# Kernel optimization log

Measured on AMD Instinct MI355X. Metric: run time of the kernel, lower is better.

Reference implementation:

```python
import jax, jax.numpy as jnp
import numpy as np
from jax import lax

T = 8192
D_MODEL = 768
D_RNN = 1024
KW = 4  # conv kernel width


def setup_inputs() -> dict:
    key = jax.random.key(0)
    ks = jax.random.split(key, 9)
    x = jax.random.normal(ks[0], (T, D_MODEL), jnp.float32)
    # equinox nn.Linear(in, out): weight [out, in], bias [out]
    w1 = jax.random.normal(ks[1], (2 * D_RNN, D_MODEL), jnp.float32) / np.sqrt(D_MODEL)
    b1 = jnp.zeros((2 * D_RNN,), jnp.float32)
    # nn.Conv1d(d_rnn, d_rnn, 4, use_bias=False): kernel [out_ch, in_ch, kw]
    conv_w = jax.random.normal(ks[2], (D_RNN, D_RNN, KW), jnp.float32) / np.sqrt(D_RNN * KW)
    w_rg = jax.random.normal(ks[3], (2 * D_RNN, D_RNN), jnp.float32) / np.sqrt(D_RNN)
    b_rg = jnp.zeros((2 * D_RNN,), jnp.float32)
    w_out = jax.random.normal(ks[4], (D_MODEL, D_RNN), jnp.float32) / np.sqrt(D_RNN)
    b_out = jnp.zeros((D_MODEL,), jnp.float32)
    # Lambda ~ U(inv_sigmoid(0.9)^{1/8}, inv_sigmoid(0.999)^{1/8}) as in __init__
    inv_sig = lambda p: np.log(1.0 / (1.0 - p))
    lower = np.power(inv_sig(0.9), 1.0 / 8.0)
    upper = np.power(inv_sig(0.999), 1.0 / 8.0)
    Lambda = jax.random.uniform(ks[5], (D_RNN,), jnp.float32, lower, upper)
    return {"x": x, "w1": w1, "b1": b1, "conv_w": conv_w, "w_rg": w_rg,
            "b_rg": b_rg, "w_out": w_out, "b_out": b_out, "Lambda": Lambda}


def _rglru_forward(x, w1, b1, conv_w, w_rg, b_rg, w_out, b_out, Lambda):
    # lin1 then split into gate branch (gelu) and recurrent branch
    h = x @ w1.T + b1                       # [T, 2*D_RNN]
    a_branch = jax.nn.gelu(h[:, :D_RNN])    # [T, D_RNN]
    b_branch = h[:, D_RNN:]                 # [T, D_RNN]
    # causal conv1d: lhs [N=1, C, T], rhs [O, I, KW], left pad 3
    bc = lax.conv_general_dilated(b_branch.T[None], conv_w, (1,), [(KW - 1, 0)])[0].T  # [T, D_RNN]
    # RG-LRU gating
    g = jax.nn.sigmoid(bc @ w_rg.T + b_rg)  # [T, 2*D_RNN]
    inp_gate = g[:, :D_RNN]
    rec_gate = g[:, D_RNN:]
    a_t = jnp.exp(-8.0 * jax.nn.softplus(Lambda)[None, :] * rec_gate)  # [T, D_RNN]
    gated_x = jnp.sqrt(1.0 - a_t ** 2) * inp_gate * bc

    def rec_step(state, xs):
        gx, av = xs
        hn = av * state + gx
        return hn, hn

    _, y = lax.scan(rec_step, jnp.zeros((D_RNN,), x.dtype), (gated_x, a_t))
    return (a_branch * y) @ w_out.T + b_out  # [T, D_MODEL]


def reference(x, w1, b1, conv_w, w_rg, b_rg, w_out, b_out, Lambda):
    return _rglru_forward(x, w1, b1, conv_w, w_rg, b_rg, w_out, b_out, Lambda)
```

## Files before the change

kernel.cpp:

```cpp
#include <hip/hip_runtime.h>
#include <hip/hip_bf16.h>
#include <stdint.h>


#define T_LEN 8192
#define DM 768
#define DR 1024
#define NC 128
#define CL 64

typedef __bf16 bf16x8 __attribute__((ext_vector_type(8)));
typedef float  f32x4  __attribute__((ext_vector_type(4)));

#define AS1 __attribute__((address_space(1)))
#define AS3 __attribute__((address_space(3)))

__device__ __forceinline__ void cp16_g2l(const void* g, void* l) {
    __builtin_amdgcn_global_load_lds((const AS1 void*)g, (AS3 void*)l, 16, 0, 0);
}

__device__ __forceinline__ float gelu_tanh(float x) {
    const float inner = 0.7978845608028654f * (x + 0.044715f * x * x * x);
    return 0.5f * x * (1.f + tanhf(inner));
}

template<int BN, int EPI, bool SHIFT>
__global__ __launch_bounds__(256, 2)
void gemm_mfma(const __hip_bfloat16* __restrict__ A,
               const __hip_bfloat16* __restrict__ B,
               const float* __restrict__ bias,
               void* __restrict__ Cv,
               int K, int lda, int N,
               __hip_bfloat16* __restrict__ D2)
{
    constexpr int NI  = BN / 32;
    constexpr int NLD = 4 + NI;
    __shared__ __bf16 As[2][128 * 64];
    __shared__ __bf16 Bs[2][BN * 64];

    const int tid  = threadIdx.x;
    const int lane = tid & 63;
    const int wave = tid >> 6;
    const size_t m0 = (size_t)blockIdx.x * 128;
    const int    n0 = blockIdx.y * BN;
    const int wm = (wave >> 1) * 64;
    const int wn = (wave & 1) * (BN / 2);

    f32x4 acc[4][NI];
#pragma unroll
    for (int i = 0; i < 4; ++i)
#pragma unroll
        for (int j = 0; j < NI; ++j)
            acc[i][j] = f32x4{0.f, 0.f, 0.f, 0.f};

    const int frow = lane & 15;
    const int fq   = lane >> 4;

    auto stage = [&](int buf, int k0) {
#pragma unroll
        for (int q = 0; q < 4; ++q) {
            const int lin = q * 256 + tid;
            const int rr  = lin >> 3;
            const int gc  = (lin & 7) ^ (rr & 7);
            const size_t ar = m0 + rr + (SHIFT ? (size_t)(k0 >> 10) : 0);
            const int    ac = SHIFT ? (k0 & 1023) : k0;
            cp16_g2l(A + ar * (size_t)lda + ac + gc * 8, &As[buf][lin * 8]);
        }
#pragma unroll
        for (int q = 0; q < NI; ++q) {
            const int lin = q * 256 + tid;
            const int rr  = lin >> 3;
            const int gc  = (lin & 7) ^ (rr & 7);
            cp16_g2l(B + (size_t)(n0 + rr) * K + k0 + gc * 8, &Bs[buf][lin * 8]);
        }
    };

    const int nt = K / 64;
    stage(0, 0);
    int cur = 0;
    for (int t = 0; t < nt; ++t) {
        if (t + 1 < nt) {
            stage(cur ^ 1, (t + 1) * 64);
            asm volatile("s_waitcnt vmcnt(%0)" :: "n"(NLD) : "memory");
        } else {
            asm volatile("s_waitcnt vmcnt(0)" ::: "memory");
        }
        __builtin_amdgcn_s_barrier();
        asm volatile("" ::: "memory");

        bf16x8 af[2][4], bfr[2][NI];
#pragma unroll
        for (int ks = 0; ks < 2; ++ks) {
#pragma unroll
            for (int mi = 0; mi < 4; ++mi) {
                const int R = wm + mi * 16 + frow;
                af[ks][mi] = *(const bf16x8*)&As[cur][R * 64 + (((ks * 4 + fq) ^ (R & 7)) * 8)];
            }
#pragma unroll
            for (int ni = 0; ni < NI; ++ni) {
                const int R = wn + ni * 16 + frow;
                bfr[ks][ni] = *(const bf16x8*)&Bs[cur][R * 64 + (((ks * 4 + fq) ^ (R & 7)) * 8)];
            }
        }
        asm volatile("s_waitcnt lgkmcnt(0)" ::: "memory");
        __builtin_amdgcn_s_barrier();
        asm volatile("" ::: "memory");

#pragma unroll
        for (int ks = 0; ks < 2; ++ks)
#pragma unroll
            for (int mi = 0; mi < 4; ++mi)
#pragma unroll
                for (int ni = 0; ni < NI; ++ni)
                    acc[mi][ni] = __builtin_amdgcn_mfma_f32_16x16x32_bf16(
                        af[ks][mi], bfr[ks][ni], acc[mi][ni], 0, 0, 0);
        cur ^= 1;
    }

    const int er = fq * 4;
    const int ec = frow;
#pragma unroll
    for (int ni = 0; ni < NI; ++ni) {
        const int n = n0 + wn + ni * 16 + ec;
        const float bv = bias ? bias[n] : 0.f;
#pragma unroll
        for (int mi = 0; mi < 4; ++mi) {
#pragma unroll
            for (int r2 = 0; r2 < 4; ++r2) {
                const size_t m = m0 + wm + mi * 16 + er + r2;
                const float v = acc[mi][ni][r2] + bv;
                if (EPI == 0) {
                    ((float*)Cv)[m * (size_t)N + n] = v;
                } else if (EPI == 1) {
                    ((__hip_bfloat16*)Cv)[m * (size_t)N + n] = __float2bfloat16(v);
                } else {
                    if (n < 1024)
                        ((__hip_bfloat16*)Cv)[m * 1024 + n] = __float2bfloat16(gelu_tanh(v));
                    else
                        D2[(m + 3) * 1024 + (n - 1024)] = __float2bfloat16(v);
                }
            }
        }
    }
}

#define PREP_X   6291456
#define PREP_W1  (PREP_X + 1572864)
#define PREP_WRG (PREP_W1 + 2097152)
#define PREP_WO  (PREP_WRG + 786432)
#define PREP_CW  (PREP_WO + 4194304)
#define PREP_TOT (PREP_CW + 3072)
__global__ void prep_kernel(const float* __restrict__ x, const float* __restrict__ w1,
                            const float* __restrict__ w_rg, const float* __restrict__ w_out,
                            const float* __restrict__ conv_w,
                            __hip_bfloat16* __restrict__ xb, __hip_bfloat16* __restrict__ w1b,
                            __hip_bfloat16* __restrict__ w_rgb, __hip_bfloat16* __restrict__ w_outb,
                            __hip_bfloat16* __restrict__ wbigb, __hip_bfloat16* __restrict__ bbp)
{
    const int idx = blockIdx.x * 256 + threadIdx.x;
    if (idx < PREP_X) {
        xb[idx] = __float2bfloat16(x[idx]);
    } else if (idx < PREP_W1) {
        const int i = idx - PREP_X;  w1b[i] = __float2bfloat16(w1[i]);
    } else if (idx < PREP_WRG) {
        const int i = idx - PREP_W1; w_rgb[i] = __float2bfloat16(w_rg[i]);
    } else if (idx < PREP_WO) {
        const int i = idx - PREP_WRG; w_outb[i] = __float2bfloat16(w_out[i]);
    } else if (idx < PREP_CW) {
        const int n = idx - PREP_WO;
        const int o = n >> 12, r = n & 4095, k = r >> 10, i = r & 1023;
        wbigb[n] = __float2bfloat16(conv_w[o * 4096 + i * 4 + k]);
    } else {
        bbp[idx - PREP_CW] = __float2bfloat16(0.f);
    }
}

__global__ void scan_pass1(const __hip_bfloat16* __restrict__ gp,
                           const __hip_bfloat16* __restrict__ bc,
                           const float* __restrict__ Lambda,
                           float* __restrict__ ch, float* __restrict__ ca)
{
    const int c = blockIdx.y * 256 + threadIdx.x;
    const int j = blockIdx.x;
    const float cl = -8.f * log1pf(expf(Lambda[c]));
    float h = 0.f, ap = 1.f;
    const int t0 = j * CL;
    for (int tt = 0; tt < CL; ++tt) {
        const int t = t0 + tt;
        const long gi = (long)t * 2048 + c;
        const float ig = 1.f / (1.f + expf(-__bfloat162float(gp[gi])));
        const float rg = 1.f / (1.f + expf(-__bfloat162float(gp[gi + 1024])));
        const float a  = expf(cl * rg);
        const float gx = sqrtf(fmaxf(0.f, 1.f - a * a)) * ig *
                         __bfloat162float(bc[(long)t * 1024 + c]);
        h  = fmaf(a, h, gx);
        ap *= a;
    }
    ch[j * 1024 + c] = h;
    ca[j * 1024 + c] = ap;
}

__global__ void scan_combine(float* __restrict__ ch, const float* __restrict__ ca)
{
    const int c = blockIdx.x * 256 + threadIdx.x;
    float carry = 0.f;
    for (int j = 0; j < NC; ++j) {
        const float hj = ch[j * 1024 + c];
        const float aj = ca[j * 1024 + c];
        ch[j * 1024 + c] = carry;
        carry = fmaf(aj, carry, hj);
    }
}

__global__ void scan_pass2(const __hip_bfloat16* __restrict__ gp, const __hip_bfloat16* bc,
                           const float* __restrict__ Lambda,
                           const float* __restrict__ carry_in,
                           const __hip_bfloat16* __restrict__ ab,
                           __hip_bfloat16* zb)
{
    const int c = blockIdx.y * 256 + threadIdx.x;
    const int j = blockIdx.x;
    const float cl = -8.f * log1pf(expf(Lambda[c]));
    float h = carry_in[j * 1024 + c];
    const int t0 = j * CL;
    for (int tt = 0; tt < CL; ++tt) {
        const int t = t0 + tt;
        const long gi = (long)t * 2048 + c;
        const long bi = (long)t * 1024 + c;
        const float ig = 1.f / (1.f + expf(-__bfloat162float(gp[gi])));
        const float rg = 1.f / (1.f + expf(-__bfloat162float(gp[gi + 1024])));
        const float a  = expf(cl * rg);
        const float gx = sqrtf(fmaxf(0.f, 1.f - a * a)) * ig * __bfloat162float(bc[bi]);
        h = fmaf(a, h, gx);
        zb[bi] = __float2bfloat16(__bfloat162float(ab[bi]) * h);
    }
}

extern "C" void kernel_launch(void* const* d_in, const int* in_sizes, int n_in,
                              void* d_out, int out_size, void* d_ws, size_t ws_size,
                              hipStream_t stream)
{
    const float* x      = (const float*)d_in[0];
    const float* w1     = (const float*)d_in[1];
    const float* b1     = (const float*)d_in[2];
    const float* conv_w = (const float*)d_in[3];
    const float* w_rg   = (const float*)d_in[4];
    const float* b_rg   = (const float*)d_in[5];
    const float* w_out  = (const float*)d_in[6];
    const float* b_out  = (const float*)d_in[7];
    const float* Lambda = (const float*)d_in[8];
    float* out = (float*)d_out;
    (void)in_sizes; (void)n_in; (void)out_size; (void)ws_size;

    char* p = (char*)d_ws;
    auto alloc = [&](size_t bytes) { char* r = p; p += (bytes + 255) & ~255ULL; return r; };
    __hip_bfloat16* gpre  = (__hip_bfloat16*)alloc(8192ULL * 2048 * 2);
    __hip_bfloat16* ab    = (__hip_bfloat16*)alloc(8192ULL * 1024 * 2);
    __hip_bfloat16* bbp   = (__hip_bfloat16*)alloc(8200ULL * 1024 * 2);
    __hip_bfloat16* bcb   = (__hip_bfloat16*)alloc(8192ULL * 1024 * 2);
    __hip_bfloat16* wbigb = (__hip_bfloat16*)alloc(1024ULL * 4096 * 2);
    __hip_bfloat16* xb    = (__hip_bfloat16*)alloc(8192ULL * 768 * 2);
    __hip_bfloat16* w1b   = (__hip_bfloat16*)alloc(2048ULL * 768 * 2);
    __hip_bfloat16* w_rgb = (__hip_bfloat16*)alloc(2048ULL * 1024 * 2);
    __hip_bfloat16* w_outb= (__hip_bfloat16*)alloc(768ULL * 1024 * 2);
    float*          chv   = (float*)alloc(NC * 1024ULL * 4);
    float*          cav   = (float*)alloc(NC * 1024ULL * 4);
    __hip_bfloat16* zb    = bcb;

    prep_kernel<<<PREP_TOT / 256, 256, 0, stream>>>(x, w1, w_rg, w_out, conv_w,
                                                    xb, w1b, w_rgb, w_outb, wbigb, bbp);

    {
        dim3 grid(T_LEN / 128, 2048 / 128);
        gemm_mfma<128, 2, false><<<grid, 256, 0, stream>>>(xb, w1b, b1, ab, DM, DM, 2048, bbp);
    }

    {
        dim3 grid(T_LEN / 128, 1024 / 128);
        gemm_mfma<128, 1, true><<<grid, 256, 0, stream>>>(bbp, wbigb, nullptr, bcb, 4096, 1024, 1024, nullptr);
    }

    {
        dim3 grid(T_LEN / 128, 2048 / 128);
        gemm_mfma<128, 1, false><<<grid, 256, 0, stream>>>(bcb, w_rgb, b_rg, gpre, DR, DR, 2048, nullptr);
    }

    {
        dim3 gs(NC, DR / 256);
        scan_pass1<<<gs, 256, 0, stream>>>(gpre, bcb, Lambda, chv, cav);
        scan_combine<<<DR / 256, 256, 0, stream>>>(chv, cav);
        scan_pass2<<<gs, 256, 0, stream>>>(gpre, bcb, Lambda, chv, ab, zb);
    }

    {
        dim3 grid(T_LEN / 128, DM / 64);
        gemm_mfma<64, 0, false><<<grid, 256, 0, stream>>>(zb, w_outb, b_out, out, DR, DR, DM, nullptr);
    }
}
```

Measured before the change: 277.7 us.

## Stage GEMM epilogue through LDS for vectorized stores, widen scan to two channels

The GEMM epilogue now writes accumulators into swizzled shared memory and then issues 16-byte row-contiguous global stores, replacing scattered per-element scalar stores. The scan kernels each handle two adjacent channels per thread using bf16x2 loads and stores, which halves the grid. Scheduling barriers are placed around the s_barrier calls. The added LDS round trip and extra syncthreads bring a small cost, and the scan now has fewer threads in flight to hide latency.

```diff
diff --git a/kernel.cpp b/kernel.cpp
--- a/kernel.cpp
+++ b/kernel.cpp
@@ -10,6 +10,7 @@
 #define CL 64
 
 typedef __bf16 bf16x8 __attribute__((ext_vector_type(8)));
+typedef __bf16 bf16x2 __attribute__((ext_vector_type(2)));
 typedef float  f32x4  __attribute__((ext_vector_type(4)));
 
 #define AS1 __attribute__((address_space(1)))
@@ -22,6 +23,15 @@
 __device__ __forceinline__ float gelu_tanh(float x) {
     const float inner = 0.7978845608028654f * (x + 0.044715f * x * x * x);
     return 0.5f * x * (1.f + tanhf(inner));
+}
+
+__device__ __forceinline__ __bf16 f2b(float v) {
+    __hip_bfloat16 h = __float2bfloat16(v);
+    return *reinterpret_cast<__bf16*>(&h);
+}
+__device__ __forceinline__ float b2f(__bf16 v) {
+    __hip_bfloat16 h = *reinterpret_cast<__hip_bfloat16*>(&v);
+    return __bfloat162float(h);
 }
 
 template<int BN, int EPI, bool SHIFT>
@@ -85,8 +95,9 @@
         } else {
             asm volatile("s_waitcnt vmcnt(0)" ::: "memory");
         }
+        __builtin_amdgcn_sched_barrier(0);
         __builtin_amdgcn_s_barrier();
-        asm volatile("" ::: "memory");
+        __builtin_amdgcn_sched_barrier(0);
 
         bf16x8 af[2][4], bfr[2][NI];
 #pragma unroll
@@ -103,8 +114,9 @@
             }
         }
         asm volatile("s_waitcnt lgkmcnt(0)" ::: "memory");
+        __builtin_amdgcn_sched_barrier(0);
         __builtin_amdgcn_s_barrier();
-        asm volatile("" ::: "memory");
+        __builtin_amdgcn_sched_barrier(0);
 
 #pragma unroll
         for (int ks = 0; ks < 2; ++ks)
@@ -117,28 +129,63 @@
         cur ^= 1;
     }
 
+    __syncthreads();
     const int er = fq * 4;
     const int ec = frow;
-#pragma unroll
-    for (int ni = 0; ni < NI; ++ni) {
-        const int n = n0 + wn + ni * 16 + ec;
-        const float bv = bias ? bias[n] : 0.f;
-#pragma unroll
-        for (int mi = 0; mi < 4; ++mi) {
-#pragma unroll
-            for (int r2 = 0; r2 < 4; ++r2) {
-                const size_t m = m0 + wm + mi * 16 + er + r2;
-                const float v = acc[mi][ni][r2] + bv;
-                if (EPI == 0) {
-                    ((float*)Cv)[m * (size_t)N + n] = v;
-                } else if (EPI == 1) {
-                    ((__hip_bfloat16*)Cv)[m * (size_t)N + n] = __float2bfloat16(v);
-                } else {
-                    if (n < 1024)
-                        ((__hip_bfloat16*)Cv)[m * 1024 + n] = __float2bfloat16(gelu_tanh(v));
-                    else
-                        D2[(m + 3) * 1024 + (n - 1024)] = __float2bfloat16(v);
+
+    if (EPI == 0) {
+        float* Cl = (float*)&As[0][0];
+#pragma unroll
+        for (int ni = 0; ni < NI; ++ni) {
+            const int cc = wn + ni * 16 + ec;
+            const float bv = bias ? bias[n0 + cc] : 0.f;
+#pragma unroll
+            for (int mi = 0; mi < 4; ++mi)
+#pragma unroll
+                for (int r2 = 0; r2 < 4; ++r2) {
+                    const int R = wm + mi * 16 + er + r2;
+                    Cl[R * 64 + ((((cc >> 2) ^ (R & 7)) << 2) | (cc & 3))] =
+                        acc[mi][ni][r2] + bv;
                 }
+        }
+        __syncthreads();
+        float* outp = (float*)Cv;
+#pragma unroll
+        for (int p = 0; p < 8; ++p) {
+            const int R   = (tid >> 4) + p * 16;
+            const int chn = tid & 15;
+            const f32x4 v = *(const f32x4*)&Cl[R * 64 + ((chn ^ (R & 7)) << 2)];
+            *(f32x4*)&outp[(m0 + R) * (size_t)N + n0 + chn * 4] = v;
+        }
+    } else {
+        __bf16* Cl = (__bf16*)&As[0][0];
+        const bool ahalf = (EPI == 2) && (n0 < 1024);
+#pragma unroll
+        for (int ni = 0; ni < NI; ++ni) {
+            const int cc = wn + ni * 16 + ec;
+            const float bv = bias ? bias[n0 + cc] : 0.f;
+#pragma unroll
+            for (int mi = 0; mi < 4; ++mi)
+#pragma unroll
+                for (int r2 = 0; r2 < 4; ++r2) {
+                    const int R = wm + mi * 16 + er + r2;
+                    float v = acc[mi][ni][r2] + bv;
+                    if (EPI == 2 && ahalf) v = gelu_tanh(v);
+                    Cl[R * 128 + ((((cc >> 3) ^ (R & 7)) << 3) | (cc & 7))] = f2b(v);
+                }
+        }
+        __syncthreads();
+#pragma unroll
+        for (int p = 0; p < 8; ++p) {
+            const int R   = (tid >> 4) + p * 16;
+            const int chn = tid & 15;
+            const bf16x8 v = *(const bf16x8*)&Cl[R * 128 + ((chn ^ (R & 7)) << 3)];
+            if (EPI == 1) {
+                *(bf16x8*)((__bf16*)Cv + (m0 + R) * (size_t)N + n0 + chn * 8) = v;
+            } else if (n0 < 1024) {
+                *(bf16x8*)((__bf16*)Cv + (m0 + R) * 1024 + n0 + chn * 8) = v;
+            } else {
+                *(bf16x8*)((__bf16*)D2 + (m0 + R + 3) * 1024 + (n0 - 1024) + chn * 8) = v;
             }
         }
     }
@@ -180,24 +227,30 @@
                            const float* __restrict__ Lambda,
                            float* __restrict__ ch, float* __restrict__ ca)
 {
-    const int c = blockIdx.y * 256 + threadIdx.x;
+    const int c = (blockIdx.y * 256 + threadIdx.x) * 2;
     const int j = blockIdx.x;
-    const float cl = -8.f * log1pf(expf(Lambda[c]));
-    float h = 0.f, ap = 1.f;
+    const float cl0 = -8.f * log1pf(expf(Lambda[c]));
+    const float cl1 = -8.f * log1pf(expf(Lambda[c + 1]));
+    float h0 = 0.f, h1 = 0.f, ap0 = 1.f, ap1 = 1.f;
     const int t0 = j * CL;
     for (int tt = 0; tt < CL; ++tt) {
         const int t = t0 + tt;
-        const long gi = (long)t * 2048 + c;
-        const float ig = 1.f / (1.f + expf(-__bfloat162float(gp[gi])));
-        const float rg = 1.f / (1.f + expf(-__bfloat162float(gp[gi + 1024])));
-        const float a  = expf(cl * rg);
-        const float gx = sqrtf(fmaxf(0.f, 1.f - a * a)) * ig *
-                         __bfloat162float(bc[(long)t * 1024 + c]);
-        h  = fmaf(a, h, gx);
-        ap *= a;
-    }
-    ch[j * 1024 + c] = h;
-    ca[j * 1024 + c] = ap;
+        const bf16x2 igv = *(const bf16x2*)&gp[(long)t * 2048 + c];
+        const bf16x2 rgv = *(const bf16x2*)&gp[(long)t * 2048 + 1024 + c];
+        const bf16x2 bcv = *(const bf16x2*)&bc[(long)t * 1024 + c];
+        const float ig0 = 1.f / (1.f + expf(-b2f(igv[0])));
+        const float ig1 = 1.f / (1.f + expf(-b2f(igv[1])));
+        const float rg0 = 1.f / (1.f + expf(-b2f(rgv[0])));
+        const float rg1 = 1.f / (1.f + expf(-b2f(rgv[1])));
+        const float a0  = expf(cl0 * rg0);
+        const float a1  = expf(cl1 * rg1);
+        const float gx0 = sqrtf(fmaxf(0.f, 1.f - a0 * a0)) * ig0 * b2f(bcv[0]);
+        const float gx1 = sqrtf(fmaxf(0.f, 1.f - a1 * a1)) * ig1 * b2f(bcv[1]);
+        h0 = fmaf(a0, h0, gx0);  ap0 *= a0;
+        h1 = fmaf(a1, h1, gx1);  ap1 *= a1;
+    }
+    ch[j * 1024 + c] = h0;  ch[j * 1024 + c + 1] = h1;
+    ca[j * 1024 + c] = ap0; ca[j * 1024 + c + 1] = ap1;
 }
 
 __global__ void scan_combine(float* __restrict__ ch, const float* __restrict__ ca)
@@ -218,21 +271,34 @@
                            const __hip_bfloat16* __restrict__ ab,
                            __hip_bfloat16* zb)
 {
-    const int c = blockIdx.y * 256 + threadIdx.x;
+    const int c = (blockIdx.y * 256 + threadIdx.x) * 2;
     const int j = blockIdx.x;
-    const float cl = -8.f * log1pf(expf(Lambda[c]));
-    float h = carry_in[j * 1024 + c];
+    const float cl0 = -8.f * log1pf(expf(Lambda[c]));
+    const float cl1 = -8.f * log1pf(expf(Lambda[c + 1]));
+    float h0 = carry_in[j * 1024 + c];
+    float h1 = carry_in[j * 1024 + c + 1];
     const int t0 = j * CL;
     for (int tt = 0; tt < CL; ++tt) {
         const int t = t0 + tt;
-        const long gi = (long)t * 2048 + c;
         const long bi = (long)t * 1024 + c;
-        const float ig = 1.f / (1.f + expf(-__bfloat162float(gp[gi])));
-        const float rg = 1.f / (1.f + expf(-__bfloat162float(gp[gi + 1024])));
-        const float a  = expf(cl * rg);
-        const float gx = sqrtf(fmaxf(0.f, 1.f - a * a)) * ig * __bfloat162float(bc[bi]);
-        h = fmaf(a, h, gx);
-        zb[bi] = __float2bfloat16(__bfloat162float(ab[bi]) * h);
+        const bf16x2 igv = *(const bf16x2*)&gp[(long)t * 2048 + c];
+        const bf16x2 rgv = *(const bf16x2*)&gp[(long)t * 2048 + 1024 + c];
+        const bf16x2 bcv = *(const bf16x2*)&bc[bi];
+        const bf16x2 abv = *(const bf16x2*)&ab[bi];
+        const float ig0 = 1.f / (1.f + expf(-b2f(igv[0])));
+        const float ig1 = 1.f / (1.f + expf(-b2f(igv[1])));
+        const float rg0 = 1.f / (1.f + expf(-b2f(rgv[0])));
+        const float rg1 = 1.f / (1.f + expf(-b2f(rgv[1])));
+        const float a0  = expf(cl0 * rg0);
+        const float a1  = expf(cl1 * rg1);
+        const float gx0 = sqrtf(fmaxf(0.f, 1.f - a0 * a0)) * ig0 * b2f(bcv[0]);
+        const float gx1 = sqrtf(fmaxf(0.f, 1.f - a1 * a1)) * ig1 * b2f(bcv[1]);
+        h0 = fmaf(a0, h0, gx0);
+        h1 = fmaf(a1, h1, gx1);
+        bf16x2 o;
+        o[0] = f2b(b2f(abv[0]) * h0);
+        o[1] = f2b(b2f(abv[1]) * h1);
+        *(bf16x2*)&zb[bi] = o;
     }
 }
 
@@ -286,7 +352,7 @@
     }
 
     {
-        dim3 gs(NC, DR / 256);
+        dim3 gs(NC, DR / 512);
         scan_pass1<<<gs, 256, 0, stream>>>(gpre, bcb, Lambda, chv, cav);
         scan_combine<<<DR / 256, 256, 0, stream>>>(chv, cav);
         scan_pass2<<<gs, 256, 0, stream>>>(gpre, bcb, Lambda, chv, ab, zb);
```

Result: slower. 298.9 us (+7.6%).

## Halve GEMM K-tile for higher occupancy and stage epilogue through LDS

Applied to the files above, without the earlier changes.

Cuts the K depth per stage of the bf16 MFMA GEMM from 64 to 32 and remaps the LDS swizzle to match, so shared memory drops to 32KB and launch bounds can allow 4 blocks per SM. Adds sched barriers and raises wave priority around the MFMA block. The epilogue now writes results into swizzled LDS and then issues coalesced 16-byte vector stores, replacing scattered scalar global stores. In exchange there are twice as many barrier/stage iterations per K, and register pressure has to fit the tighter launch bound.

```diff
diff --git a/kernel.cpp b/kernel.cpp
--- a/kernel.cpp
+++ b/kernel.cpp
@@ -24,8 +24,13 @@
     return 0.5f * x * (1.f + tanhf(inner));
 }
 
+__device__ __forceinline__ __bf16 f2b(float v) {
+    __hip_bfloat16 h = __float2bfloat16(v);
+    return *reinterpret_cast<__bf16*>(&h);
+}
+
 template<int BN, int EPI, bool SHIFT>
-__global__ __launch_bounds__(256, 2)
+__global__ __launch_bounds__(256, 4)
 void gemm_mfma(const __hip_bfloat16* __restrict__ A,
                const __hip_bfloat16* __restrict__ B,
                const float* __restrict__ bias,
@@ -34,9 +39,11 @@
                __hip_bfloat16* __restrict__ D2)
 {
     constexpr int NI  = BN / 32;
-    constexpr int NLD = 4 + NI;
-    __shared__ __bf16 As[2][128 * 64];
-    __shared__ __bf16 Bs[2][BN * 64];
+    constexpr int BLD = (BN * 4) / 256;
+    constexpr int NLD = 2 + BLD;
+    __shared__ __align__(16) unsigned char smem[32768];
+    __bf16* Asb = (__bf16*)smem;
+    __bf16* Bsb = (__bf16*)(smem + 16384);
 
     const int tid  = threadIdx.x;
     const int lane = tid & 63;
@@ -58,87 +65,122 @@
 
     auto stage = [&](int buf, int k0) {
 #pragma unroll
-        for (int q = 0; q < 4; ++q) {
+        for (int q = 0; q < 2; ++q) {
             const int lin = q * 256 + tid;
-            const int rr  = lin >> 3;
-            const int gc  = (lin & 7) ^ (rr & 7);
+            const int rr  = lin >> 2;
+            const int gc  = (lin & 3) ^ ((rr >> 1) & 3);
             const size_t ar = m0 + rr + (SHIFT ? (size_t)(k0 >> 10) : 0);
             const int    ac = SHIFT ? (k0 & 1023) : k0;
-            cp16_g2l(A + ar * (size_t)lda + ac + gc * 8, &As[buf][lin * 8]);
-        }
-#pragma unroll
-        for (int q = 0; q < NI; ++q) {
+            cp16_g2l(A + ar * (size_t)lda + ac + gc * 8, Asb + buf * 4096 + lin * 8);
+        }
+#pragma unroll
+        for (int q = 0; q < BLD; ++q) {
             const int lin = q * 256 + tid;
-            const int rr  = lin >> 3;
-            const int gc  = (lin & 7) ^ (rr & 7);
-            cp16_g2l(B + (size_t)(n0 + rr) * K + k0 + gc * 8, &Bs[buf][lin * 8]);
+            const int rr  = lin >> 2;
+            const int gc  = (lin & 3) ^ ((rr >> 1) & 3);
+            cp16_g2l(B + (size_t)(n0 + rr) * K + k0 + gc * 8,
+                     Bsb + buf * (BN * 32) + lin * 8);
         }
     };
 
-    const int nt = K / 64;
+    const int nt = K / 32;
     stage(0, 0);
     int cur = 0;
     for (int t = 0; t < nt; ++t) {
         if (t + 1 < nt) {
-            stage(cur ^ 1, (t + 1) * 64);
+            stage(cur ^ 1, (t + 1) * 32);
             asm volatile("s_waitcnt vmcnt(%0)" :: "n"(NLD) : "memory");
         } else {
             asm volatile("s_waitcnt vmcnt(0)" ::: "memory");
         }
+        __builtin_amdgcn_sched_barrier(0);
         __builtin_amdgcn_s_barrier();
-        asm volatile("" ::: "memory");
-
-        bf16x8 af[2][4], bfr[2][NI];
-#pragma unroll
-        for (int ks = 0; ks < 2; ++ks) {
-#pragma unroll
-            for (int mi = 0; mi < 4; ++mi) {
-                const int R = wm + mi * 16 + frow;
-                af[ks][mi] = *(const bf16x8*)&As[cur][R * 64 + (((ks * 4 + fq) ^ (R & 7)) * 8)];
-            }
-#pragma unroll
-            for (int ni = 0; ni < NI; ++ni) {
-                const int R = wn + ni * 16 + frow;
-                bfr[ks][ni] = *(const bf16x8*)&Bs[cur][R * 64 + (((ks * 4 + fq) ^ (R & 7)) * 8)];
-            }
+        __builtin_amdgcn_sched_barrier(0);
+
+        bf16x8 af[4], bfr[NI];
+#pragma unroll
+        for (int mi = 0; mi < 4; ++mi) {
+            const int R = wm + mi * 16 + frow;
+            af[mi] = *(const bf16x8*)&Asb[cur * 4096 + R * 32 + ((fq ^ ((R >> 1) & 3)) * 8)];
+        }
+#pragma unroll
+        for (int ni = 0; ni < NI; ++ni) {
+            const int R = wn + ni * 16 + frow;
+            bfr[ni] = *(const bf16x8*)&Bsb[cur * (BN * 32) + R * 32 + ((fq ^ ((R >> 1) & 3)) * 8)];
         }
         asm volatile("s_waitcnt lgkmcnt(0)" ::: "memory");
+        __builtin_amdgcn_sched_barrier(0);
         __builtin_amdgcn_s_barrier();
-        asm volatile("" ::: "memory");
-
-#pragma unroll
-        for (int ks = 0; ks < 2; ++ks)
-#pragma unroll
-            for (int mi = 0; mi < 4; ++mi)
-#pragma unroll
-                for (int ni = 0; ni < NI; ++ni)
-                    acc[mi][ni] = __builtin_amdgcn_mfma_f32_16x16x32_bf16(
-                        af[ks][mi], bfr[ks][ni], acc[mi][ni], 0, 0, 0);
+        __builtin_amdgcn_sched_barrier(0);
+
+        __builtin_amdgcn_s_setprio(1);
+#pragma unroll
+        for (int mi = 0; mi < 4; ++mi)
+#pragma unroll
+            for (int ni = 0; ni < NI; ++ni)
+                acc[mi][ni] = __builtin_amdgcn_mfma_f32_16x16x32_bf16(
+                    af[mi], bfr[ni], acc[mi][ni], 0, 0, 0);
+        __builtin_amdgcn_s_setprio(0);
         cur ^= 1;
     }
 
+    __syncthreads();
     const int er = fq * 4;
     const int ec = frow;
-#pragma unroll
-    for (int ni = 0; ni < NI; ++ni) {
-        const int n = n0 + wn + ni * 16 + ec;
-        const float bv = bias ? bias[n] : 0.f;
-#pragma unroll
-        for (int mi = 0; mi < 4; ++mi) {
-#pragma unroll
-            for (int r2 = 0; r2 < 4; ++r2) {
-                const size_t m = m0 + wm + mi * 16 + er + r2;
-                const float v = acc[mi][ni][r2] + bv;
-                if (EPI == 0) {
-                    ((float*)Cv)[m * (size_t)N + n] = v;
-                } else if (EPI == 1) {
-                    ((__hip_bfloat16*)Cv)[m * (size_t)N + n] = __float2bfloat16(v);
-                } else {
-                    if (n < 1024)
-                        ((__hip_bfloat16*)Cv)[m * 1024 + n] = __float2bfloat16(gelu_tanh(v));
-                    else
-                        D2[(m + 3) * 1024 + (n - 1024)] = __float2bfloat16(v);
+
+    if (EPI == 0) {
+        float* Cl = (float*)smem;
+#pragma unroll
+        for (int ni = 0; ni < NI; ++ni) {
+            const int cc = wn + ni * 16 + ec;
+            const float bv = bias ? bias[n0 + cc] : 0.f;
+#pragma unroll
+            for (int mi = 0; mi < 4; ++mi)
+#pragma unroll
+                for (int r2 = 0; r2 < 4; ++r2) {
+                    const int R = wm + mi * 16 + er + r2;
+                    Cl[R * 64 + ((((cc >> 2) ^ (R & 7)) << 2) | (cc & 3))] =
+                        acc[mi][ni][r2] + bv;
                 }
+        }
+        __syncthreads();
+        float* outp = (float*)Cv;
+#pragma unroll
+        for (int p = 0; p < 8; ++p) {
+            const int R   = (tid >> 4) + p * 16;
+            const int chn = tid & 15;
+            const f32x4 v = *(const f32x4*)&Cl[R * 64 + ((chn ^ (R & 7)) << 2)];
+            *(f32x4*)&outp[(m0 + R) * (size_t)N + n0 + chn * 4] = v;
+        }
+    } else {
+        __bf16* Cl = (__bf16*)smem;
+        const bool ahalf = (EPI == 2) && (n0 < 1024);
+#pragma unroll
+        for (int ni = 0; ni < NI; ++ni) {
+            const int cc = wn + ni * 16 + ec;
+            const float bv = bias ? bias[n0 + cc] : 0.f;
+#pragma unroll
+            for (int mi = 0; mi < 4; ++mi)
+#pragma unroll
+                for (int r2 = 0; r2 < 4; ++r2) {
+                    const int R = wm + mi * 16 + er + r2;
+                    float v = acc[mi][ni][r2] + bv;
+                    if (EPI == 2 && ahalf) v = gelu_tanh(v);
+                    Cl[R * 128 + ((((cc >> 3) ^ (R & 7)) << 3) | (cc & 7))] = f2b(v);
+                }
+        }
+        __syncthreads();
+#pragma unroll
+        for (int p = 0; p < 8; ++p) {
+            const int R   = (tid >> 4) + p * 16;
+            const int chn = tid & 15;
+            const bf16x8 v = *(const bf16x8*)&Cl[R * 128 + ((chn ^ (R & 7)) << 3)];
+            if (EPI == 1) {
+                *(bf16x8*)((__bf16*)Cv + (m0 + R) * (size_t)N + n0 + chn * 8) = v;
+            } else if (n0 < 1024) {
+                *(bf16x8*)((__bf16*)Cv + (m0 + R) * 1024 + n0 + chn * 8) = v;
+            } else {
+                *(bf16x8*)((__bf16*)D2 + (m0 + R + 3) * 1024 + (n0 - 1024) + chn * 8) = v;
             }
         }
     }
```

After: 284.0 us. +2.3%, slower.
